# Optimization experiments

Hardware: AMD Instinct MI355X
Metric: run time of the kernel (lower is better)

The kernel has to match this reference:

```python
import jax, jax.numpy as jnp
import numpy as np

B, S, D, H = 2, 2048, 1024, 16
HD = D // H  # head_dim = 64

def setup_inputs() -> dict:
    key = jax.random.key(0)
    ks = jax.random.split(key, 10)
    s = 1.0 / np.sqrt(D)
    return {
        "hidden_states": jax.random.normal(ks[0], (B, S, D), jnp.float32),
        "attention_mask": jnp.ones((B, S), jnp.float32),
        "q_w": jax.random.uniform(ks[1], (D, D), jnp.float32, -s, s),
        "q_b": jax.random.uniform(ks[2], (D,), jnp.float32, -s, s),
        "k_w": jax.random.uniform(ks[3], (D, D), jnp.float32, -s, s),
        "k_b": jax.random.uniform(ks[4], (D,), jnp.float32, -s, s),
        "v_w": jax.random.uniform(ks[5], (D, D), jnp.float32, -s, s),
        "v_b": jax.random.uniform(ks[6], (D,), jnp.float32, -s, s),
        "o_w": jax.random.uniform(ks[7], (D, D), jnp.float32, -s, s),
        "o_b": jax.random.uniform(ks[8], (D,), jnp.float32, -s, s),
    }

def reference(hidden_states, attention_mask, q_w, q_b, k_w, k_b, v_w, v_b, o_w, o_b):
    scale = HD ** -0.5
    # projections; torch Linear: x @ W^T + b. Here weights stored as (D, D) used directly.
    q = hidden_states @ q_w + q_b  # [B,S,D]
    k = hidden_states @ k_w + k_b
    v = hidden_states @ v_w + v_b
    # split heads -> [B,H,S,HD]
    q = q.reshape(B, S, H, HD).transpose(0, 2, 1, 3)
    k = k.reshape(B, S, H, HD).transpose(0, 2, 1, 3)
    v = v.reshape(B, S, H, HD).transpose(0, 2, 1, 3)
    scores = jnp.einsum('bhqd,bhkd->bhqk', q, k) * scale  # [B,H,S,S]
    # additive mask from 2D [B,S] mask (1=keep, 0=mask)
    scores = scores + (1.0 - attention_mask)[:, None, None, :] * -10000.0
    attn = jax.nn.softmax(scores, axis=-1)
    ctx = jnp.einsum('bhqk,bhkd->bhqd', attn, v)  # [B,H,S,HD]
    ctx = ctx.transpose(0, 2, 1, 3).reshape(B, S, D)
    return ctx @ o_w + o_b
```

## Files before the change

kernel.cpp:

```cpp
#include <hip/hip_runtime.h>
#include <hip/hip_bf16.h>

#define B_ 2
#define S_ 2048
#define D_ 1024
#define H_ 16
#define HD_ 64

#define QSCALE 0.18033688f
#define MLOG2E 14426.950408f

typedef __attribute__((ext_vector_type(8))) short bf16x8;
typedef __attribute__((ext_vector_type(4))) short short4v;
typedef __attribute__((ext_vector_type(4))) float floatx4;

static __device__ __forceinline__ float bf2f(short u) {
  union { float f; unsigned int i; } c;
  c.i = ((unsigned int)(unsigned short)u) << 16;
  return c.f;
}
static __device__ __forceinline__ short f2bf(float f) {
  union { float f; unsigned int i; } c; c.f = f;
  unsigned int r = c.i + 0x7FFFu + ((c.i >> 16) & 1u);
  return (short)(r >> 16);
}
static __device__ __forceinline__ short f2bf_fast(float f) {
  union { float f; unsigned int i; } c; c.f = f;
  return (short)((c.i + 0x8000u) >> 16);
}

static __device__ __forceinline__ void gld_lds16(const void* g, void* l) {
  __builtin_amdgcn_global_load_lds(
      (const __attribute__((address_space(1))) unsigned int*)g,
      (__attribute__((address_space(3))) unsigned int*)l, 16, 0, 0);
}

__global__ __launch_bounds__(256)
void prep(const float* __restrict__ w0, const float* __restrict__ w1,
          const float* __restrict__ w2, const float* __restrict__ w3,
          const float* __restrict__ hs, short* __restrict__ WT,
          short* __restrict__ Xb) {
  const int z = blockIdx.z;
  if (z < 4) {
    __shared__ short t[64][65];
    const float* src = z == 0 ? w0 : z == 1 ? w1 : z == 2 ? w2 : w3;
    short* dst = WT + (size_t)z * D_ * D_;
    const int tx = threadIdx.x & 63, ty = threadIdx.x >> 6;
    const int r0 = blockIdx.y * 64, c0 = blockIdx.x * 64;
    for (int r = ty; r < 64; r += 4)
      t[r][tx] = f2bf(src[(size_t)(r0 + r) * D_ + c0 + tx]);
    __syncthreads();
    for (int r = ty; r < 64; r += 4)
      dst[(size_t)(c0 + r) * D_ + r0 + tx] = t[tx][r];
  } else {
    const int bid = blockIdx.y * 16 + blockIdx.x;
    const float4* in4 = (const float4*)hs;
    short4v* out4 = (short4v*)Xb;
#pragma unroll
    for (int i = 0; i < 16; i++) {
      const int idx = bid * 4096 + i * 256 + threadIdx.x;
      const float4 v = in4[idx];
      short4v o;
      o[0] = f2bf(v.x); o[1] = f2bf(v.y); o[2] = f2bf(v.z); o[3] = f2bf(v.w);
      out4[idx] = o;
    }
  }
}

__global__ __launch_bounds__(256, 3)
void gemm_qkv(const short* __restrict__ X, const short* __restrict__ WT,
              const float* __restrict__ qb, const float* __restrict__ kb,
              const float* __restrict__ vb,
              short* __restrict__ Qo, short* __restrict__ Ko,
              short* __restrict__ Vt) {
  __shared__ __align__(16) short As[128 * 32];
  __shared__ __align__(16) short Bs[128 * 32];
  const int tid = threadIdx.x;
  const int wave = tid >> 6, lane = tid & 63;
  const int col = lane & 15, quad = lane >> 4;
  const int m0 = blockIdx.x * 128;
  const int nt = blockIdx.y;
  const int widx = nt >> 3;
  const int n1 = (nt & 7) * 128;
  const short* Bsrc = WT + (size_t)widx * D_ * D_ + (size_t)n1 * D_;
  const int b = m0 >> 11;

  const int srow = tid >> 2;
  const int skcol = (tid & 3) * 8;
  const short* ga = X + (size_t)(m0 + srow) * D_ + skcol;
  const short* gb = Bsrc + (size_t)srow * D_ + skcol;
  short* la = As + tid * 8;
  short* lb = Bs + tid * 8;

  floatx4 acc[4][4];
#pragma unroll
  for (int i = 0; i < 4; i++)
#pragma unroll
    for (int j = 0; j < 4; j++) acc[i][j] = floatx4{0.f, 0.f, 0.f, 0.f};

  if (widx < 2) {
    const int wseq = (wave >> 1) * 64;
    const int wfeat = (wave & 1) * 64;
    for (int k0 = 0; k0 < D_; k0 += 32) {
      gld_lds16(ga, la);
      gld_lds16(ga + 64 * D_, la + 2048);
      gld_lds16(gb, lb);
      gld_lds16(gb + 64 * D_, lb + 2048);
      ga += 32; gb += 32;
      __syncthreads();
      bf16x8 xf[4], wf[4];
#pragma unroll
      for (int j = 0; j < 4; j++)
        xf[j] = *(const bf16x8*)(As + (wseq + j * 16 + col) * 32 + quad * 8);
#pragma unroll
      for (int i = 0; i < 4; i++)
        wf[i] = *(const bf16x8*)(Bs + (wfeat + i * 16 + col) * 32 + quad * 8);
#pragma unroll
      for (int i = 0; i < 4; i++)
#pragma unroll
        for (int j = 0; j < 4; j++)
          acc[i][j] = __builtin_amdgcn_mfma_f32_16x16x32_bf16(wf[i], xf[j],
                                                              acc[i][j], 0, 0, 0);
      __syncthreads();
    }
    const float* bias = widx == 0 ? qb : kb;
    short* dst = widx == 0 ? Qo : Ko;
    const float scale = widx == 0 ? QSCALE : 1.0f;
#pragma unroll
    for (int i = 0; i < 4; i++) {
      const int nf = n1 + wfeat + i * 16 + quad * 4;
      const int h = nf >> 6, hd = nf & 63;
      const float4 bv = *(const float4*)(bias + nf);
#pragma unroll
      for (int j = 0; j < 4; j++) {
        const int s = (m0 + wseq + j * 16 + col) & (S_ - 1);
        short4v pk;
        pk[0] = f2bf((acc[i][j][0] + bv.x) * scale);
        pk[1] = f2bf((acc[i][j][1] + bv.y) * scale);
        pk[2] = f2bf((acc[i][j][2] + bv.z) * scale);
        pk[3] = f2bf((acc[i][j][3] + bv.w) * scale);
        *(short4v*)(dst + ((size_t)(b * H_ + h) * S_ + s) * HD_ + hd) = pk;
      }
    }
  } else {
    const int wrow = (wave & 1) * 64;
    const int wcol = (wave >> 1) * 64;
    for (int k0 = 0; k0 < D_; k0 += 32) {
      gld_lds16(ga, la);
      gld_lds16(ga + 64 * D_, la + 2048);
      gld_lds16(gb, lb);
      gld_lds16(gb + 64 * D_, lb + 2048);
      ga += 32; gb += 32;
      __syncthreads();
      bf16x8 af[4], bfr[4];
#pragma unroll
      for (int i = 0; i < 4; i++)
        af[i] = *(const bf16x8*)(As + (wrow + i * 16 + col) * 32 + quad * 8);
#pragma unroll
      for (int j = 0; j < 4; j++)
        bfr[j] = *(const bf16x8*)(Bs + (wcol + j * 16 + col) * 32 + quad * 8);
#pragma unroll
      for (int i = 0; i < 4; i++)
#pragma unroll
        for (int j = 0; j < 4; j++)
          acc[i][j] = __builtin_amdgcn_mfma_f32_16x16x32_bf16(af[i], bfr[j],
                                                              acc[i][j], 0, 0, 0);
      __syncthreads();
    }
    float bv[4];
#pragma unroll
    for (int j = 0; j < 4; j++) bv[j] = vb[n1 + wcol + j * 16 + col];
#pragma unroll
    for (int i = 0; i < 4; i++) {
      const int s = (m0 + wrow + i * 16 + quad * 4) & (S_ - 1);
#pragma unroll
      for (int j = 0; j < 4; j++) {
        const int nl = n1 + wcol + j * 16 + col;
        const int h = nl >> 6, hd = nl & 63;
        short4v pk;
#pragma unroll
        for (int r = 0; r < 4; r++) pk[r] = f2bf(acc[i][j][r] + bv[j]);
        *(short4v*)(Vt + ((size_t)(b * H_ + h) * HD_ + hd) * S_ + s) = pk;
      }
    }
  }
}

__global__ __launch_bounds__(256, 2)
void attn(const short* __restrict__ Q, const short* __restrict__ K,
          const short* __restrict__ Vt, const float* __restrict__ mask,
          short* __restrict__ ctx) {
  __shared__ __align__(16) short Ks[2][4096];
  __shared__ __align__(16) short Vs[2][4096];
  __shared__ __align__(16) short P[4][2][16][68];
  const int tid = threadIdx.x, wave = tid >> 6, lane = tid & 63;
  const int col = lane & 15, quad = lane >> 4;
  const int qt = blockIdx.x, h = blockIdx.y, b = blockIdx.z;
  const short* Qh = Q + (size_t)(b * H_ + h) * S_ * HD_;
  const short* Kh = K + (size_t)(b * H_ + h) * S_ * HD_;
  const short* Vh = Vt + (size_t)(b * H_ + h) * HD_ * S_;
  const float* mk = mask + (size_t)b * S_;
  const int q0 = qt * 128 + wave * 32;

  const int r1 = tid >> 3, c1 = (tid & 7) ^ (r1 & 7);
  const int r2 = r1 + 32,  c2 = (tid & 7) ^ (r2 & 7);
  const int swz = quad ^ (col & 7);

  gld_lds16(Kh + (size_t)r1 * HD_ + c1 * 8, &Ks[0][tid * 8]);
  gld_lds16(Kh + (size_t)r2 * HD_ + c2 * 8, &Ks[0][(tid + 256) * 8]);
  gld_lds16(Vh + (size_t)r1 * S_ + c1 * 8, &Vs[0][tid * 8]);
  gld_lds16(Vh + (size_t)r2 * S_ + c2 * 8, &Vs[0][(tid + 256) * 8]);

  bf16x8 qf[2][2];
#pragma unroll
  for (int g = 0; g < 2; g++) {
    const short* qp = Qh + (size_t)(q0 + g * 16 + col) * HD_;
    qf[g][0] = *(const bf16x8*)(qp + quad * 8);
    qf[g][1] = *(const bf16x8*)(qp + 32 + quad * 8);
  }

  bf16x8 ones;
#pragma unroll
  for (int i = 0; i < 8; i++) ones[i] = (short)0x3F80;

  floatx4 acc[2][4], rsacc[2];
#pragma unroll
  for (int g = 0; g < 2; g++) {
    rsacc[g] = floatx4{0.f, 0.f, 0.f, 0.f};
#pragma unroll
    for (int d = 0; d < 4; d++) acc[g][d] = floatx4{0.f, 0.f, 0.f, 0.f};
  }

  __syncthreads();

  for (int it = 0; it < S_ / 64; it++) {
    const int buf = it & 1;
    const int kt = it * 64;
    if (it + 1 < S_ / 64) {
      const int kn = kt + 64;
      gld_lds16(Kh + (size_t)(kn + r1) * HD_ + c1 * 8, &Ks[buf ^ 1][tid * 8]);
      gld_lds16(Kh + (size_t)(kn + r2) * HD_ + c2 * 8, &Ks[buf ^ 1][(tid + 256) * 8]);
      gld_lds16(Vh + (size_t)r1 * S_ + kn + c1 * 8, &Vs[buf ^ 1][tid * 8]);
      gld_lds16(Vh + (size_t)r2 * S_ + kn + c2 * 8, &Vs[buf ^ 1][(tid + 256) * 8]);
    }

    float m2v[4];
#pragma unroll
    for (int t = 0; t < 4; t++)
      m2v[t] = mk[kt + t * 16 + col] * MLOG2E - MLOG2E;

    bf16x8 kf[4][2];
#pragma unroll
    for (int t = 0; t < 4; t++) {
      const short* kp = &Ks[buf][(t * 16 + col) * 64];
      kf[t][0] = *(const bf16x8*)(kp + swz * 8);
      kf[t][1] = *(const bf16x8*)(kp + (swz ^ 4) * 8);
    }

#pragma unroll
    for (int g = 0; g < 2; g++)
#pragma unroll
      for (int t = 0; t < 4; t++) {
        floatx4 z = floatx4{0.f, 0.f, 0.f, 0.f};
        z = __builtin_amdgcn_mfma_f32_16x16x32_bf16(qf[g][0], kf[t][0], z, 0, 0, 0);
        z = __builtin_amdgcn_mfma_f32_16x16x32_bf16(qf[g][1], kf[t][1], z, 0, 0, 0);
#pragma unroll
        for (int r = 0; r < 4; r++)
          P[wave][g][quad * 4 + r][t * 16 + col] = f2bf_fast(exp2f(z[r] + m2v[t]));
      }

    bf16x8 pf[2][2];
#pragma unroll
    for (int g = 0; g < 2; g++)
#pragma unroll
      for (int kk = 0; kk < 2; kk++) {
        const short4v p0 = *(const short4v*)&P[wave][g][col][kk * 32 + quad * 8];
        const short4v p1 = *(const short4v*)&P[wave][g][col][kk * 32 + quad * 8 + 4];
        bf16x8 pv;
        pv[0] = p0[0]; pv[1] = p0[1]; pv[2] = p0[2]; pv[3] = p0[3];
        pv[4] = p1[0]; pv[5] = p1[1]; pv[6] = p1[2]; pv[7] = p1[3];
        pf[g][kk] = pv;
      }

#pragma unroll
    for (int g = 0; g < 2; g++) {
      rsacc[g] = __builtin_amdgcn_mfma_f32_16x16x32_bf16(ones, pf[g][0], rsacc[g], 0, 0, 0);
      rsacc[g] = __builtin_amdgcn_mfma_f32_16x16x32_bf16(ones, pf[g][1], rsacc[g], 0, 0, 0);
    }
#pragma unroll
    for (int d = 0; d < 4; d++) {
      const short* vp = &Vs[buf][(d * 16 + col) * 64];
      const bf16x8 vf0 = *(const bf16x8*)(vp + swz * 8);
      const bf16x8 vf1 = *(const bf16x8*)(vp + (swz ^ 4) * 8);
#pragma unroll
      for (int g = 0; g < 2; g++) {
        acc[g][d] = __builtin_amdgcn_mfma_f32_16x16x32_bf16(vf0, pf[g][0], acc[g][d], 0, 0, 0);
        acc[g][d] = __builtin_amdgcn_mfma_f32_16x16x32_bf16(vf1, pf[g][1], acc[g][d], 0, 0, 0);
      }
    }
    __syncthreads();
  }

#pragma unroll
  for (int g = 0; g < 2; g++) {
    const float inv = 1.0f / (rsacc[g][0] + 1e-30f);
    const size_t row = (size_t)b * S_ + q0 + g * 16 + col;
#pragma unroll
    for (int d = 0; d < 4; d++) {
      short4v o;
#pragma unroll
      for (int r = 0; r < 4; r++) o[r] = f2bf(acc[g][d][r] * inv);
      *(short4v*)(ctx + row * D_ + h * HD_ + d * 16 + quad * 4) = o;
    }
  }
}

__global__ __launch_bounds__(256, 2)
void gemm_out(const short* __restrict__ X, const short* __restrict__ WT,
              const float* __restrict__ ob, float* __restrict__ out) {
  __shared__ __align__(16) short As[128 * 32];
  __shared__ __align__(16) short Bs[128 * 32];
  const int tid = threadIdx.x;
  const int wave = tid >> 6, lane = tid & 63;
  const int col = lane & 15, quad = lane >> 4;
  const int m0 = blockIdx.x * 128;
  const int n0 = blockIdx.y * 128;
  const short* Bsrc = WT + (size_t)n0 * D_;
  const int wrow = (wave & 1) * 64;
  const int wcol = (wave >> 1) * 64;

  floatx4 acc[4][4];
#pragma unroll
  for (int i = 0; i < 4; i++)
#pragma unroll
    for (int j = 0; j < 4; j++) acc[i][j] = floatx4{0.f, 0.f, 0.f, 0.f};

  const int srow = tid >> 2;
  const int skcol = (tid & 3) * 8;
  const short* ga = X + (size_t)(m0 + srow) * D_ + skcol;
  const short* gb = Bsrc + (size_t)srow * D_ + skcol;
  short* la = As + tid * 8;
  short* lb = Bs + tid * 8;

  for (int k0 = 0; k0 < D_; k0 += 32) {
    gld_lds16(ga, la);
    gld_lds16(ga + 64 * D_, la + 2048);
    gld_lds16(gb, lb);
    gld_lds16(gb + 64 * D_, lb + 2048);
    ga += 32; gb += 32;
    __syncthreads();
    bf16x8 af[4], bfr[4];
#pragma unroll
    for (int i = 0; i < 4; i++)
      af[i] = *(const bf16x8*)(As + (wrow + i * 16 + col) * 32 + quad * 8);
#pragma unroll
    for (int j = 0; j < 4; j++)
      bfr[j] = *(const bf16x8*)(Bs + (wcol + j * 16 + col) * 32 + quad * 8);
#pragma unroll
    for (int i = 0; i < 4; i++)
#pragma unroll
      for (int j = 0; j < 4; j++)
        acc[i][j] = __builtin_amdgcn_mfma_f32_16x16x32_bf16(af[i], bfr[j],
                                                            acc[i][j], 0, 0, 0);
    __syncthreads();
  }

  float bv[4];
#pragma unroll
  for (int j = 0; j < 4; j++) bv[j] = ob[n0 + wcol + j * 16 + col];

#pragma unroll
  for (int i = 0; i < 4; i++) {
    const int m = m0 + wrow + i * 16 + quad * 4;
#pragma unroll
    for (int j = 0; j < 4; j++) {
      const int n = n0 + wcol + j * 16 + col;
#pragma unroll
      for (int r = 0; r < 4; r++)
        out[(size_t)(m + r) * D_ + n] = acc[i][j][r] + bv[j];
    }
  }
}

extern "C" void kernel_launch(void* const* d_in, const int* in_sizes, int n_in,
                              void* d_out, int out_size, void* d_ws, size_t ws_size,
                              hipStream_t stream) {
  (void)in_sizes; (void)n_in; (void)out_size; (void)ws_size;
  const float* hs  = (const float*)d_in[0];
  const float* msk = (const float*)d_in[1];
  const float* qw  = (const float*)d_in[2];
  const float* qb  = (const float*)d_in[3];
  const float* kw  = (const float*)d_in[4];
  const float* kb  = (const float*)d_in[5];
  const float* vw  = (const float*)d_in[6];
  const float* vb  = (const float*)d_in[7];
  const float* ow  = (const float*)d_in[8];
  const float* ob  = (const float*)d_in[9];
  float* out = (float*)d_out;
  char* ws = (char*)d_ws;

  short* Xb  = (short*)(ws);
  short* WT  = (short*)(ws + (8ull  << 20));
  short* Qp  = (short*)(ws + (16ull << 20));
  short* Kp  = (short*)(ws + (24ull << 20));
  short* Vtp = (short*)(ws + (32ull << 20));
  short* Ctx = Xb;

  prep<<<dim3(16, 16, 5), 256, 0, stream>>>(qw, kw, vw, ow, hs, WT, Xb);
  gemm_qkv<<<dim3(32, 24), 256, 0, stream>>>(Xb, WT, qb, kb, vb, Qp, Kp, Vtp);
  attn<<<dim3(16, 16, 2), 256, 0, stream>>>(Qp, Kp, Vtp, msk, Ctx);
  gemm_out<<<dim3(32, 8), 256, 0, stream>>>(Ctx, WT + 3ull * D_ * D_, ob, out);
}
```

Before: 227.5 us.

## Fold mask into V and row-sum weights, transpose score MFMA, retile out GEMM

The mask is no longer added to the scores inside the attention loop. Instead its weight exp((m-1)*c) multiplies V rows in the QKV epilogue and weights the row-sum MFMA through a shared-memory table, which removes the per-tile mask loads and adds. The score MFMA operands are swapped so each lane writes a packed short4 to P and reads back a bf16x8 in one load, with P padded to 72. The attention grid is linearised so consecutive blocks map to different heads, and the output GEMM uses 64-row tiles for twice as many blocks. Factoring the mask out of exp this way relies on the scores staying small without max subtraction, which the kernel already assumed.

```diff
diff --git a/kernel.cpp b/kernel.cpp
--- a/kernel.cpp
+++ b/kernel.cpp
@@ -70,7 +70,7 @@
 __global__ __launch_bounds__(256, 3)
 void gemm_qkv(const short* __restrict__ X, const short* __restrict__ WT,
               const float* __restrict__ qb, const float* __restrict__ kb,
-              const float* __restrict__ vb,
+              const float* __restrict__ vb, const float* __restrict__ mask,
               short* __restrict__ Qo, short* __restrict__ Ko,
               short* __restrict__ Vt) {
   __shared__ __align__(16) short As[128 * 32];
@@ -170,16 +170,23 @@
     float bv[4];
 #pragma unroll
     for (int j = 0; j < 4; j++) bv[j] = vb[n1 + wcol + j * 16 + col];
+    const float* mkb = mask + (size_t)b * S_;
 #pragma unroll
     for (int i = 0; i < 4; i++) {
       const int s = (m0 + wrow + i * 16 + quad * 4) & (S_ - 1);
+      const float4 mv = *(const float4*)(mkb + s);
+      float w[4];
+      w[0] = exp2f((mv.x - 1.0f) * MLOG2E);
+      w[1] = exp2f((mv.y - 1.0f) * MLOG2E);
+      w[2] = exp2f((mv.z - 1.0f) * MLOG2E);
+      w[3] = exp2f((mv.w - 1.0f) * MLOG2E);
 #pragma unroll
       for (int j = 0; j < 4; j++) {
         const int nl = n1 + wcol + j * 16 + col;
         const int h = nl >> 6, hd = nl & 63;
         short4v pk;
 #pragma unroll
-        for (int r = 0; r < 4; r++) pk[r] = f2bf(acc[i][j][r] + bv[j]);
+        for (int r = 0; r < 4; r++) pk[r] = f2bf((acc[i][j][r] + bv[j]) * w[r]);
         *(short4v*)(Vt + ((size_t)(b * H_ + h) * HD_ + hd) * S_ + s) = pk;
       }
     }
@@ -192,10 +199,14 @@
           short* __restrict__ ctx) {
   __shared__ __align__(16) short Ks[2][4096];
   __shared__ __align__(16) short Vs[2][4096];
-  __shared__ __align__(16) short P[4][2][16][68];
+  __shared__ __align__(16) short P[4][2][16][72];
+  __shared__ __align__(16) short Ws[S_];
   const int tid = threadIdx.x, wave = tid >> 6, lane = tid & 63;
   const int col = lane & 15, quad = lane >> 4;
-  const int qt = blockIdx.x, h = blockIdx.y, b = blockIdx.z;
+  const int lin = blockIdx.x;
+  const int qt = (lin >> 3) & 15;
+  const int gi = (lin & 7) + ((lin >> 7) << 3);
+  const int h = gi & 15, b = gi >> 4;
   const short* Qh = Q + (size_t)(b * H_ + h) * S_ * HD_;
   const short* Kh = K + (size_t)(b * H_ + h) * S_ * HD_;
   const short* Vh = Vt + (size_t)(b * H_ + h) * HD_ * S_;
@@ -211,6 +222,9 @@
   gld_lds16(Vh + (size_t)r1 * S_ + c1 * 8, &Vs[0][tid * 8]);
   gld_lds16(Vh + (size_t)r2 * S_ + c2 * 8, &Vs[0][(tid + 256) * 8]);
 
+  for (int i = tid; i < S_; i += 256)
+    Ws[i] = f2bf(exp2f((mk[i] - 1.0f) * MLOG2E));
+
   bf16x8 qf[2][2];
 #pragma unroll
   for (int g = 0; g < 2; g++) {
@@ -218,10 +232,6 @@
     qf[g][0] = *(const bf16x8*)(qp + quad * 8);
     qf[g][1] = *(const bf16x8*)(qp + 32 + quad * 8);
   }
-
-  bf16x8 ones;
-#pragma unroll
-  for (int i = 0; i < 8; i++) ones[i] = (short)0x3F80;
 
   floatx4 acc[2][4], rsacc[2];
 #pragma unroll
@@ -244,11 +254,6 @@
       gld_lds16(Vh + (size_t)r2 * S_ + kn + c2 * 8, &Vs[buf ^ 1][(tid + 256) * 8]);
     }
 
-    float m2v[4];
-#pragma unroll
-    for (int t = 0; t < 4; t++)
-      m2v[t] = mk[kt + t * 16 + col] * MLOG2E - MLOG2E;
-
     bf16x8 kf[4][2];
 #pragma unroll
     for (int t = 0; t < 4; t++) {
@@ -262,30 +267,30 @@
 #pragma unroll
       for (int t = 0; t < 4; t++) {
         floatx4 z = floatx4{0.f, 0.f, 0.f, 0.f};
-        z = __builtin_amdgcn_mfma_f32_16x16x32_bf16(qf[g][0], kf[t][0], z, 0, 0, 0);
-        z = __builtin_amdgcn_mfma_f32_16x16x32_bf16(qf[g][1], kf[t][1], z, 0, 0, 0);
-#pragma unroll
-        for (int r = 0; r < 4; r++)
-          P[wave][g][quad * 4 + r][t * 16 + col] = f2bf_fast(exp2f(z[r] + m2v[t]));
+        z = __builtin_amdgcn_mfma_f32_16x16x32_bf16(kf[t][0], qf[g][0], z, 0, 0, 0);
+        z = __builtin_amdgcn_mfma_f32_16x16x32_bf16(kf[t][1], qf[g][1], z, 0, 0, 0);
+        short4v pk;
+#pragma unroll
+        for (int r = 0; r < 4; r++) pk[r] = f2bf_fast(exp2f(z[r]));
+        *(short4v*)&P[wave][g][col][t * 16 + quad * 4] = pk;
       }
 
     bf16x8 pf[2][2];
 #pragma unroll
     for (int g = 0; g < 2; g++)
 #pragma unroll
-      for (int kk = 0; kk < 2; kk++) {
-        const short4v p0 = *(const short4v*)&P[wave][g][col][kk * 32 + quad * 8];
-        const short4v p1 = *(const short4v*)&P[wave][g][col][kk * 32 + quad * 8 + 4];
-        bf16x8 pv;
-        pv[0] = p0[0]; pv[1] = p0[1]; pv[2] = p0[2]; pv[3] = p0[3];
-        pv[4] = p1[0]; pv[5] = p1[1]; pv[6] = p1[2]; pv[7] = p1[3];
-        pf[g][kk] = pv;
-      }
+      for (int kk = 0; kk < 2; kk++)
+        pf[g][kk] = *(const bf16x8*)&P[wave][g][col][kk * 32 + quad * 8];
+
+    bf16x8 wf[2];
+#pragma unroll
+    for (int kk = 0; kk < 2; kk++)
+      wf[kk] = *(const bf16x8*)&Ws[kt + kk * 32 + quad * 8];
 
 #pragma unroll
     for (int g = 0; g < 2; g++) {
-      rsacc[g] = __builtin_amdgcn_mfma_f32_16x16x32_bf16(ones, pf[g][0], rsacc[g], 0, 0, 0);
-      rsacc[g] = __builtin_amdgcn_mfma_f32_16x16x32_bf16(ones, pf[g][1], rsacc[g], 0, 0, 0);
+      rsacc[g] = __builtin_amdgcn_mfma_f32_16x16x32_bf16(wf[0], pf[g][0], rsacc[g], 0, 0, 0);
+      rsacc[g] = __builtin_amdgcn_mfma_f32_16x16x32_bf16(wf[1], pf[g][1], rsacc[g], 0, 0, 0);
     }
 #pragma unroll
     for (int d = 0; d < 4; d++) {
@@ -318,46 +323,44 @@
 __global__ __launch_bounds__(256, 2)
 void gemm_out(const short* __restrict__ X, const short* __restrict__ WT,
               const float* __restrict__ ob, float* __restrict__ out) {
-  __shared__ __align__(16) short As[128 * 32];
+  __shared__ __align__(16) short As[64 * 32];
   __shared__ __align__(16) short Bs[128 * 32];
   const int tid = threadIdx.x;
   const int wave = tid >> 6, lane = tid & 63;
   const int col = lane & 15, quad = lane >> 4;
-  const int m0 = blockIdx.x * 128;
+  const int m0 = blockIdx.x * 64;
   const int n0 = blockIdx.y * 128;
   const short* Bsrc = WT + (size_t)n0 * D_;
-  const int wrow = (wave & 1) * 64;
+  const int wrow = (wave & 1) * 32;
   const int wcol = (wave >> 1) * 64;
 
-  floatx4 acc[4][4];
-#pragma unroll
-  for (int i = 0; i < 4; i++)
+  floatx4 acc[2][4];
+#pragma unroll
+  for (int i = 0; i < 2; i++)
 #pragma unroll
     for (int j = 0; j < 4; j++) acc[i][j] = floatx4{0.f, 0.f, 0.f, 0.f};
 
-  const int srow = tid >> 2;
-  const int skcol = (tid & 3) * 8;
-  const short* ga = X + (size_t)(m0 + srow) * D_ + skcol;
-  const short* gb = Bsrc + (size_t)srow * D_ + skcol;
+  const int arow = tid >> 2, akcol = (tid & 3) * 8;
+  const short* ga = X + (size_t)(m0 + arow) * D_ + akcol;
+  const short* gb = Bsrc + (size_t)arow * D_ + akcol;
   short* la = As + tid * 8;
   short* lb = Bs + tid * 8;
 
   for (int k0 = 0; k0 < D_; k0 += 32) {
     gld_lds16(ga, la);
-    gld_lds16(ga + 64 * D_, la + 2048);
     gld_lds16(gb, lb);
     gld_lds16(gb + 64 * D_, lb + 2048);
     ga += 32; gb += 32;
     __syncthreads();
-    bf16x8 af[4], bfr[4];
-#pragma unroll
-    for (int i = 0; i < 4; i++)
+    bf16x8 af[2], bfr[4];
+#pragma unroll
+    for (int i = 0; i < 2; i++)
       af[i] = *(const bf16x8*)(As + (wrow + i * 16 + col) * 32 + quad * 8);
 #pragma unroll
     for (int j = 0; j < 4; j++)
       bfr[j] = *(const bf16x8*)(Bs + (wcol + j * 16 + col) * 32 + quad * 8);
 #pragma unroll
-    for (int i = 0; i < 4; i++)
+    for (int i = 0; i < 2; i++)
 #pragma unroll
       for (int j = 0; j < 4; j++)
         acc[i][j] = __builtin_amdgcn_mfma_f32_16x16x32_bf16(af[i], bfr[j],
@@ -370,7 +373,7 @@
   for (int j = 0; j < 4; j++) bv[j] = ob[n0 + wcol + j * 16 + col];
 
 #pragma unroll
-  for (int i = 0; i < 4; i++) {
+  for (int i = 0; i < 2; i++) {
     const int m = m0 + wrow + i * 16 + quad * 4;
 #pragma unroll
     for (int j = 0; j < 4; j++) {
@@ -407,7 +410,7 @@
   short* Ctx = Xb;
 
   prep<<<dim3(16, 16, 5), 256, 0, stream>>>(qw, kw, vw, ow, hs, WT, Xb);
-  gemm_qkv<<<dim3(32, 24), 256, 0, stream>>>(Xb, WT, qb, kb, vb, Qp, Kp, Vtp);
-  attn<<<dim3(16, 16, 2), 256, 0, stream>>>(Qp, Kp, Vtp, msk, Ctx);
-  gemm_out<<<dim3(32, 8), 256, 0, stream>>>(Ctx, WT + 3ull * D_ * D_, ob, out);
-}
+  gemm_qkv<<<dim3(32, 24), 256, 0, stream>>>(Xb, WT, qb, kb, vb, msk, Qp, Kp, Vtp);
+  attn<<<dim3(512), 256, 0, stream>>>(Qp, Kp, Vtp, msk, Ctx);
+  gemm_out<<<dim3(64, 8), 256, 0, stream>>>(Ctx, WT + 3ull * D_ * D_, ob, out);
+}
```

Result: faster. 212.6 us (-6.5%).
